# Kernel optimization log

Measured on AMD Instinct MI355X. Metric: run time of the kernel, lower is better.

## Reference

```python
import jax, jax.numpy as jnp
import numpy as np

DIM = 768
H = 12
HD = DIM // H
LAMBDA_INIT = 0.1
EPS = 1e-6


def setup_inputs() -> dict:
    key = jax.random.key(0)
    ks = jax.random.split(key, 6)
    B, N = 2, 2048
    x = jax.random.normal(ks[0], (B, N, DIM), dtype=jnp.float32)
    xpos = jnp.broadcast_to(jnp.arange(N, dtype=jnp.int64), (B, N))
    s = 1.0 / np.sqrt(DIM)
    W_qkv1 = jax.random.normal(ks[1], (DIM, 3 * DIM), dtype=jnp.float32) * s
    W_qkv2 = jax.random.normal(ks[2], (DIM, 3 * DIM), dtype=jnp.float32) * s
    W_proj = jax.random.normal(ks[3], (DIM, DIM), dtype=jnp.float32) * s
    b_proj = jnp.zeros((DIM,), dtype=jnp.float32)
    norm_w = jnp.ones((DIM,), dtype=jnp.float32)
    lambda_1 = jnp.ones((H,), dtype=jnp.float32)
    # layer_idx=0, max_layer=12 -> scale = 1/12
    lambda_2 = jnp.full((H,), 1.0 - LAMBDA_INIT * (1.0 / 12.0), dtype=jnp.float32)
    return {"x": x, "W_qkv1": W_qkv1, "W_qkv2": W_qkv2, "W_proj": W_proj,
            "b_proj": b_proj, "norm_w": norm_w, "lambda_1": lambda_1,
            "lambda_2": lambda_2, "xpos": xpos}


def _qkv(x, W):
    B, N, C = x.shape
    qkv = (x @ W).reshape(B, N, 3, H, HD).transpose(2, 0, 3, 1, 4)  # [3,B,H,N,D]
    return qkv[0], qkv[1], qkv[2]


def reference(x, W_qkv1, W_qkv2, W_proj, b_proj, norm_w, lambda_1, lambda_2, xpos):
    B, N, C = x.shape
    scale = HD ** -0.5
    q1, k1, v1 = _qkv(x, W_qkv1)
    q2, k2, v2 = _qkv(x, W_qkv2)
    attn1 = jax.nn.softmax(jnp.einsum('bhnd,bhmd->bhnm', q1, k1) * scale, axis=-1)
    attn2 = jax.nn.softmax(jnp.einsum('bhnd,bhmd->bhnm', q2, k2) * scale, axis=-1)
    lam = (lambda_1 - lambda_2 + LAMBDA_INIT)[None, :, None, None]
    diff_attn = attn1 - lam * attn2
    out = jnp.einsum('bhnm,bhmd->bhnd', diff_attn, v1)
    out = out.transpose(0, 2, 1, 3).reshape(B, N, C)
    # RMSNorm (computed in fp32, matching torch module)
    o32 = out.astype(jnp.float32)
    rms = jax.lax.rsqrt(jnp.mean(o32 * o32, axis=-1, keepdims=True) + EPS)
    out = (o32 * rms * norm_w).astype(out.dtype)
    return out @ W_proj + b_proj
```

## Files before the change

kernel.cpp:

```cpp
#include <hip/hip_runtime.h>
#include <hip/hip_bf16.h>
#include <math.h>

#define DIMC 768
#define NH   12
#define HDIM 64
#define NSEQ 2048
#define NB   2
#define LAMBDA_INIT 0.1f

typedef __attribute__((ext_vector_type(8))) short bf16x8;
typedef __attribute__((ext_vector_type(4))) float f32x4;
typedef unsigned short u16;

__device__ __forceinline__ u16 f2b(float f) {
    unsigned u = __float_as_uint(f);
    return (u16)((u + 0x7FFFu + ((u >> 16) & 1u)) >> 16);
}
__device__ __forceinline__ float b2f(u16 h) {
    return __uint_as_float((unsigned)h << 16);
}

__global__ __launch_bounds__(256)
void split32(const float* __restrict__ x, u16* __restrict__ hi,
             u16* __restrict__ lo, int n4)
{
    for (int i = blockIdx.x * 256 + threadIdx.x; i < n4; i += gridDim.x * 256) {
        float4 v = ((const float4*)x)[i];
        ushort4 h, l;
        h.x = f2b(v.x); l.x = f2b(v.x - b2f(h.x));
        h.y = f2b(v.y); l.y = f2b(v.y - b2f(h.y));
        h.z = f2b(v.z); l.z = f2b(v.z - b2f(h.z));
        h.w = f2b(v.w); l.w = f2b(v.w - b2f(h.w));
        ((ushort4*)hi)[i] = h;
        ((ushort4*)lo)[i] = l;
    }
}

__global__ __launch_bounds__(256)
void tsplit(const float* __restrict__ src, int R, int C_ld,
            u16* __restrict__ dhi, u16* __restrict__ dlo)
{
    __shared__ float T[64][65];
    const int tid = threadIdx.x;
    const int c0 = blockIdx.x * 64, r0 = blockIdx.y * 64;
    const int row = tid >> 2, cq = (tid & 3) * 4;
#pragma unroll
    for (int it = 0; it < 4; ++it) {
        int col = cq + it * 16;
        float4 v = *(const float4*)&src[(size_t)(r0 + row) * C_ld + c0 + col];
        T[row][col+0] = v.x; T[row][col+1] = v.y;
        T[row][col+2] = v.z; T[row][col+3] = v.w;
    }
    __syncthreads();
    const int c = tid >> 2, rq = (tid & 3) * 4;
#pragma unroll
    for (int it = 0; it < 4; ++it) {
        int rr = rq + it * 16;
#pragma unroll
        for (int i = 0; i < 4; ++i) {
            float f = T[rr + i][c];
            u16 h = f2b(f);
            size_t o = (size_t)(c0 + c) * R + r0 + rr + i;
            dhi[o] = h;
            dlo[o] = f2b(f - b2f(h));
        }
    }
}

template<int MODE>
__global__ __launch_bounds__(256)
void gemm_bf16(const u16* __restrict__ Ahi, const u16* __restrict__ Alo,
               const float* __restrict__ A32,
               const u16* __restrict__ Bhi, const u16* __restrict__ Blo,
               u16* __restrict__ Qo, u16* __restrict__ Ko,
               u16* __restrict__ Vhi, u16* __restrict__ Vlo,
               float* __restrict__ OUT,
               const float* __restrict__ rrms, const float* __restrict__ normw,
               const float* __restrict__ bias)
{
    __shared__ u16 AhS[128][40], AlS[128][40], BhS[128][40], BlS[128][40];
    const int tid = threadIdx.x;
    const int l = tid & 63, w = tid >> 6;
    const int wm = w >> 1, wn = w & 1;
    const int m0 = blockIdx.y * 128, n0 = blockIdx.x * 128;
    const int srow = tid >> 1, scg = (tid & 1) * 16;

    float rsc = 1.0f;
    if (MODE == 2) rsc = rrms[m0 + srow];

    f32x4 acc[4][4];
#pragma unroll
    for (int i = 0; i < 4; ++i)
#pragma unroll
        for (int j = 0; j < 4; ++j) acc[i][j] = (f32x4){0.f,0.f,0.f,0.f};

    for (int k0 = 0; k0 < DIMC; k0 += 32) {
        if (MODE < 2) {
            const u16* pa = Ahi + (size_t)(m0 + srow) * DIMC + k0 + scg;
            const u16* pl = Alo + (size_t)(m0 + srow) * DIMC + k0 + scg;
            *(bf16x8*)&AhS[srow][scg]     = *(const bf16x8*)pa;
            *(bf16x8*)&AhS[srow][scg + 8] = *(const bf16x8*)(pa + 8);
            *(bf16x8*)&AlS[srow][scg]     = *(const bf16x8*)pl;
            *(bf16x8*)&AlS[srow][scg + 8] = *(const bf16x8*)(pl + 8);
        } else {
            const float* pa = A32 + (size_t)(m0 + srow) * DIMC + k0 + scg;
            float4 v0 = *(const float4*)(pa);
            float4 v1 = *(const float4*)(pa + 4);
            float4 v2 = *(const float4*)(pa + 8);
            float4 v3 = *(const float4*)(pa + 12);
            float4 w0 = *(const float4*)(normw + k0 + scg);
            float4 w1 = *(const float4*)(normw + k0 + scg + 4);
            float4 w2 = *(const float4*)(normw + k0 + scg + 8);
            float4 w3 = *(const float4*)(normw + k0 + scg + 12);
            float vv[16] = {v0.x,v0.y,v0.z,v0.w, v1.x,v1.y,v1.z,v1.w,
                            v2.x,v2.y,v2.z,v2.w, v3.x,v3.y,v3.z,v3.w};
            float nn[16] = {w0.x,w0.y,w0.z,w0.w, w1.x,w1.y,w1.z,w1.w,
                            w2.x,w2.y,w2.z,w2.w, w3.x,w3.y,w3.z,w3.w};
#pragma unroll
            for (int i = 0; i < 16; ++i) {
                float f = vv[i] * rsc * nn[i];
                u16 h = f2b(f);
                AhS[srow][scg + i] = h;
                AlS[srow][scg + i] = f2b(f - b2f(h));
            }
        }
        {
            const u16* pb = Bhi + (size_t)(n0 + srow) * DIMC + k0 + scg;
            const u16* pl = Blo + (size_t)(n0 + srow) * DIMC + k0 + scg;
            *(bf16x8*)&BhS[srow][scg]     = *(const bf16x8*)pb;
            *(bf16x8*)&BhS[srow][scg + 8] = *(const bf16x8*)(pb + 8);
            *(bf16x8*)&BlS[srow][scg]     = *(const bf16x8*)pl;
            *(bf16x8*)&BlS[srow][scg + 8] = *(const bf16x8*)(pl + 8);
        }
        __syncthreads();

        bf16x8 ah[4], al[4], bh[4], bl[4];
#pragma unroll
        for (int i = 0; i < 4; ++i) {
            ah[i] = *(const bf16x8*)&AhS[wm*64 + i*16 + (l & 15)][(l >> 4) * 8];
            al[i] = *(const bf16x8*)&AlS[wm*64 + i*16 + (l & 15)][(l >> 4) * 8];
            bh[i] = *(const bf16x8*)&BhS[wn*64 + i*16 + (l & 15)][(l >> 4) * 8];
            bl[i] = *(const bf16x8*)&BlS[wn*64 + i*16 + (l & 15)][(l >> 4) * 8];
        }
#pragma unroll
        for (int mi = 0; mi < 4; ++mi)
#pragma unroll
            for (int ni = 0; ni < 4; ++ni) {
                acc[mi][ni] = __builtin_amdgcn_mfma_f32_16x16x32_bf16(ah[mi], bh[ni], acc[mi][ni], 0, 0, 0);
                acc[mi][ni] = __builtin_amdgcn_mfma_f32_16x16x32_bf16(ah[mi], bl[ni], acc[mi][ni], 0, 0, 0);
                acc[mi][ni] = __builtin_amdgcn_mfma_f32_16x16x32_bf16(al[mi], bh[ni], acc[mi][ni], 0, 0, 0);
            }
        __syncthreads();
    }

#pragma unroll
    for (int mi = 0; mi < 4; ++mi) {
#pragma unroll
        for (int ni = 0; ni < 4; ++ni) {
#pragma unroll
            for (int r = 0; r < 4; ++r) {
                const int m = m0 + wm*64 + mi*16 + (l >> 4) * 4 + r;
                const int n = n0 + wn*64 + ni*16 + (l & 15);
                float val = acc[mi][ni][r];
                if (MODE == 2) {
                    OUT[(size_t)m * DIMC + n] = val + bias[n];
                } else {
                    const int three = n / DIMC;
                    const int rem = n - three * DIMC;
                    const int h = rem >> 6, d = rem & 63;
                    const int b_ = m >> 11, n_ = m & (NSEQ - 1);
                    const size_t o = ((size_t)(b_ * NH + h) * NSEQ + n_) * HDIM + d;
                    if (three == 0)      Qo[o] = f2b(val * 0.125f);
                    else if (three == 1) Ko[o] = f2b(val);
                    else {
                        u16 h16 = f2b(val);
                        Vhi[o] = h16;
                        Vlo[o] = f2b(val - b2f(h16));
                    }
                }
            }
        }
    }
}

#define KVB 64
#define NT  (NSEQ / KVB)

__global__ __launch_bounds__(256)
void attn_mfma3(const u16* __restrict__ Q1, const u16* __restrict__ K1,
                const u16* __restrict__ Vhi, const u16* __restrict__ Vlo,
                const u16* __restrict__ Q2, const u16* __restrict__ K2,
                const float* __restrict__ lam1, const float* __restrict__ lam2,
                float* __restrict__ out)
{
    __shared__ u16 K1s[KVB * 64];
    __shared__ u16 K2s[KVB * 64];
    __shared__ unsigned VtHiU[64 * 36];
    __shared__ unsigned VtLoU[64 * 36];
    __shared__ unsigned PsU[2][4][16 * 36];

    const int tid = threadIdx.x;
    const int l = tid & 63, w = tid >> 6;
    const int qt = blockIdx.x, bh = blockIdx.y;
    const int b = bh / NH, h = bh % NH;
    const size_t hoff = (size_t)bh * NSEQ * HDIM;

    const int qrow = qt * 64 + w * 16 + (l & 15);
    const u16* q1p = Q1 + hoff + (size_t)qrow * HDIM + ((l >> 4) * 8);
    const u16* q2p = Q2 + hoff + (size_t)qrow * HDIM + ((l >> 4) * 8);
    bf16x8 qa1[2], qa2[2];
#pragma unroll
    for (int hf = 0; hf < 2; ++hf) {
        qa1[hf] = *(const bf16x8*)(q1p + hf * 32);
        qa2[hf] = *(const bf16x8*)(q2p + hf * 32);
    }

    f32x4 o1[4], o2[4];
    float m1[4], l1s[4], m2[4], l2s[4];
#pragma unroll
    for (int i = 0; i < 4; ++i) {
        o1[i] = (f32x4){0.f,0.f,0.f,0.f};
        o2[i] = (f32x4){0.f,0.f,0.f,0.f};
        m1[i] = -INFINITY; m2[i] = -INFINITY; l1s[i] = 0.f; l2s[i] = 0.f;
    }

    const u16* k1p = K1 + hoff;
    const u16* k2p = K2 + hoff;
    const u16* vhp = Vhi + hoff;
    const u16* vlp = Vlo + hoff;

    const int sr  = tid >> 2;
    const int scu = (tid & 3) * 16;
    const int swz = (sr & 7) << 4;
    const int vp_ = tid & 31;
    const int vdb = (tid >> 5) * 8;

    bf16x8 pk1[2], pk2[2], pvh[2], pvl[2];

#define LOADREGS(KT)                                                           \
    {                                                                          \
        const size_t gk = (size_t)((KT) * KVB + sr) * HDIM + scu;              \
        pk1[0] = *(const bf16x8*)(k1p + gk);                                   \
        pk1[1] = *(const bf16x8*)(k1p + gk + 8);                               \
        pk2[0] = *(const bf16x8*)(k2p + gk);                                   \
        pk2[1] = *(const bf16x8*)(k2p + gk + 8);                               \
        const size_t gv = (size_t)((KT) * KVB + 2 * vp_) * HDIM + vdb;         \
        pvh[0] = *(const bf16x8*)(vhp + gv);                                   \
        pvh[1] = *(const bf16x8*)(vhp + gv + HDIM);                            \
        pvl[0] = *(const bf16x8*)(vlp + gv);                                   \
        pvl[1] = *(const bf16x8*)(vlp + gv + HDIM);                            \
    }

    LOADREGS(0)

    for (int kt = 0; kt < NT; ++kt) {
        __syncthreads();
#pragma unroll
        for (int i = 0; i < 2; ++i) {
            const int bc = (scu + i * 8) * 2;
            *(bf16x8*)((char*)K1s + sr * 128 + (bc ^ swz)) = pk1[i];
            *(bf16x8*)((char*)K2s + sr * 128 + (bc ^ swz)) = pk2[i];
        }
#pragma unroll
        for (int j = 0; j < 8; ++j) {
            VtHiU[(vdb + j) * 36 + vp_] =
                (unsigned)(u16)pvh[0][j] | ((unsigned)(u16)pvh[1][j] << 16);
            VtLoU[(vdb + j) * 36 + vp_] =
                (unsigned)(u16)pvl[0][j] | ((unsigned)(u16)pvl[1][j] << 16);
        }
        __syncthreads();

        if (kt + 1 < NT) LOADREGS(kt + 1)

        f32x4 s1[4], s2[4];
#pragma unroll
        for (int s = 0; s < 4; ++s) {
            s1[s] = (f32x4){0.f,0.f,0.f,0.f};
            s2[s] = (f32x4){0.f,0.f,0.f,0.f};
        }
        const int xr = (l & 7) << 4;
#pragma unroll
        for (int hf = 0; hf < 2; ++hf) {
            const int d0b = ((l >> 4) << 4) + (hf << 6);
#pragma unroll
            for (int s = 0; s < 4; ++s) {
                const int ra = s * 16 + (l & 15);
                bf16x8 kb1 = *(const bf16x8*)((const char*)K1s + ra * 128 + (d0b ^ xr));
                bf16x8 kb2 = *(const bf16x8*)((const char*)K2s + ra * 128 + (d0b ^ xr));
                s1[s] = __builtin_amdgcn_mfma_f32_16x16x32_bf16(qa1[hf], kb1, s1[s], 0, 0, 0);
                s2[s] = __builtin_amdgcn_mfma_f32_16x16x32_bf16(qa2[hf], kb2, s2[s], 0, 0, 0);
            }
        }

        unsigned* pw1 = &PsU[0][w][0];
        unsigned* pw2 = &PsU[1][w][0];
#pragma unroll
        for (int r = 0; r < 4; ++r) {
            const int row = (l >> 4) * 4 + r;
            float rm1 = fmaxf(fmaxf(s1[0][r], s1[1][r]), fmaxf(s1[2][r], s1[3][r]));
            float rm2 = fmaxf(fmaxf(s2[0][r], s2[1][r]), fmaxf(s2[2][r], s2[3][r]));
#pragma unroll
            for (int mm = 1; mm < 16; mm <<= 1) {
                rm1 = fmaxf(rm1, __shfl_xor(rm1, mm));
                rm2 = fmaxf(rm2, __shfl_xor(rm2, mm));
            }
            float mn1 = fmaxf(m1[r], rm1), mn2 = fmaxf(m2[r], rm2);
            float c1 = __expf(m1[r] - mn1), c2 = __expf(m2[r] - mn2);
            u16 h1[4], h2v[4];
            float rs1 = 0.f, rs2 = 0.f;
#pragma unroll
            for (int s = 0; s < 4; ++s) {
                h1[s]  = f2b(__expf(s1[s][r] - mn1));
                h2v[s] = f2b(__expf(s2[s][r] - mn2));
                rs1 += b2f(h1[s]);
                rs2 += b2f(h2v[s]);
            }
#pragma unroll
            for (int mm = 1; mm < 16; mm <<= 1) {
                rs1 += __shfl_xor(rs1, mm);
                rs2 += __shfl_xor(rs2, mm);
            }
            l1s[r] = l1s[r] * c1 + rs1;  m1[r] = mn1;
            l2s[r] = l2s[r] * c2 + rs2;  m2[r] = mn2;
#pragma unroll
            for (int dt = 0; dt < 4; ++dt) { o1[dt][r] *= c1; o2[dt][r] *= c2; }

            int x1[4], x2[4];
#pragma unroll
            for (int s = 0; s < 4; ++s) {
                x1[s] = __shfl_xor((int)h1[s], 1);
                x2[s] = __shfl_xor((int)h2v[s], 1);
            }
            const int u = l & 15;
            if ((l & 1) == 0) {
                pw1[row*36 +      (u >> 1)] = (unsigned)h1[0]  | ((unsigned)x1[0] << 16);
                pw1[row*36 + 16 + (u >> 1)] = (unsigned)h1[2]  | ((unsigned)x1[2] << 16);
                pw2[row*36 +      (u >> 1)] = (unsigned)h2v[0] | ((unsigned)x2[0] << 16);
                pw2[row*36 + 16 + (u >> 1)] = (unsigned)h2v[2] | ((unsigned)x2[2] << 16);
            } else {
                pw1[row*36 +  8 + (u >> 1)] = (unsigned)x1[1]  | ((unsigned)h1[1] << 16);
                pw1[row*36 + 24 + (u >> 1)] = (unsigned)x1[3]  | ((unsigned)h1[3] << 16);
                pw2[row*36 +  8 + (u >> 1)] = (unsigned)x2[1]  | ((unsigned)h2v[1] << 16);
                pw2[row*36 + 24 + (u >> 1)] = (unsigned)x2[3]  | ((unsigned)h2v[3] << 16);
            }
        }

#pragma unroll
        for (int h2 = 0; h2 < 2; ++h2) {
            const int po = (l & 15) * 144 + h2 * 64 + ((l >> 4) << 4);
            bf16x8 pa = *(const bf16x8*)((const char*)pw1 + po);
            bf16x8 pb = *(const bf16x8*)((const char*)pw2 + po);
#pragma unroll
            for (int dt = 0; dt < 4; ++dt) {
                const int vo = (dt * 16 + (l & 15)) * 144 + h2 * 64 + ((l >> 4) << 4);
                bf16x8 vhib = *(const bf16x8*)((const char*)VtHiU + vo);
                bf16x8 vlob = *(const bf16x8*)((const char*)VtLoU + vo);
                o1[dt] = __builtin_amdgcn_mfma_f32_16x16x32_bf16(pa, vhib, o1[dt], 0, 0, 0);
                o1[dt] = __builtin_amdgcn_mfma_f32_16x16x32_bf16(pa, vlob, o1[dt], 0, 0, 0);
                o2[dt] = __builtin_amdgcn_mfma_f32_16x16x32_bf16(pb, vhib, o2[dt], 0, 0, 0);
                o2[dt] = __builtin_amdgcn_mfma_f32_16x16x32_bf16(pb, vlob, o2[dt], 0, 0, 0);
            }
        }
    }
#undef LOADREGS

    const float lam = lam1[h] - lam2[h] + LAMBDA_INIT;
#pragma unroll
    for (int r = 0; r < 4; ++r) {
        const float i1 = 1.0f / l1s[r];
        const float i2 = lam / l2s[r];
        const int q = qt * 64 + w * 16 + (l >> 4) * 4 + r;
        const size_t rowoff = (size_t)(b * NSEQ + q) * DIMC + h * HDIM;
#pragma unroll
        for (int dt = 0; dt < 4; ++dt)
            out[rowoff + dt * 16 + (l & 15)] = o1[dt][r] * i1 - o2[dt][r] * i2;
    }
}

__global__ __launch_bounds__(256)
void rrms_kernel(const float* __restrict__ X, float* __restrict__ R)
{
    const int r = blockIdx.x;
    const int t = threadIdx.x;
    const float* row = X + (size_t)r * DIMC;
    float s = 0.f;
#pragma unroll
    for (int k = 0; k < 3; ++k) {
        float v = row[t + k * 256];
        s = fmaf(v, v, s);
    }
#pragma unroll
    for (int mm = 1; mm < 64; mm <<= 1) s += __shfl_xor(s, mm);
    __shared__ float wsum[4];
    if ((t & 63) == 0) wsum[t >> 6] = s;
    __syncthreads();
    if (t == 0) R[r] = rsqrtf((wsum[0]+wsum[1]+wsum[2]+wsum[3]) * (1.0f/DIMC) + 1e-6f);
}

extern "C" void kernel_launch(void* const* d_in, const int* in_sizes, int n_in,
                              void* d_out, int out_size, void* d_ws, size_t ws_size,
                              hipStream_t stream)
{
    const float* x   = (const float*)d_in[0];
    const float* Wq1 = (const float*)d_in[1];
    const float* Wq2 = (const float*)d_in[2];
    const float* Wp  = (const float*)d_in[3];
    const float* bp  = (const float*)d_in[4];
    const float* nw  = (const float*)d_in[5];
    const float* la1 = (const float*)d_in[6];
    const float* la2 = (const float*)d_in[7];
    float* out = (float*)d_out;

    const size_t HSZ = (size_t)NB * NH * NSEQ * HDIM;
    const size_t XSZ = (size_t)NB * NSEQ * DIMC;

    u16* p = (u16*)d_ws;
    u16* Q1b = p;  p += HSZ;
    u16* K1b = p;  p += HSZ;
    u16* Q2b = p;  p += HSZ;
    u16* K2b = p;  p += HSZ;
    u16* V1h = p;  p += HSZ;
    u16* V1l = p;  p += HSZ;
    u16* xhi = p;  p += XSZ;
    u16* xlo = p;  p += XSZ;
    u16* W1th = p; p += (size_t)2304 * 768;
    u16* W1tl = p; p += (size_t)2304 * 768;
    u16* W2th = p; p += (size_t)1536 * 768;
    u16* W2tl = p; p += (size_t)1536 * 768;
    u16* Wpth = p; p += (size_t)768 * 768;
    u16* Wptl = p; p += (size_t)768 * 768;
    float* AO = (float*)p;
    float* RR = AO + XSZ;

    split32<<<dim3(1024), 256, 0, stream>>>(x, xhi, xlo, (int)(XSZ / 4));
    tsplit<<<dim3(36, 12), 256, 0, stream>>>(Wq1, DIMC, 3*DIMC, W1th, W1tl);
    tsplit<<<dim3(24, 12), 256, 0, stream>>>(Wq2, DIMC, 3*DIMC, W2th, W2tl);
    tsplit<<<dim3(12, 12), 256, 0, stream>>>(Wp,  DIMC, DIMC,   Wpth, Wptl);

    gemm_bf16<0><<<dim3(18, 32), 256, 0, stream>>>(xhi, xlo, nullptr, W1th, W1tl,
                                                   Q1b, K1b, V1h, V1l, nullptr,
                                                   nullptr, nullptr, nullptr);
    gemm_bf16<1><<<dim3(12, 32), 256, 0, stream>>>(xhi, xlo, nullptr, W2th, W2tl,
                                                   Q2b, K2b, nullptr, nullptr, nullptr,
                                                   nullptr, nullptr, nullptr);
    attn_mfma3<<<dim3(NSEQ/64, NB*NH), 256, 0, stream>>>(Q1b, K1b, V1h, V1l,
                                                         Q2b, K2b, la1, la2, AO);
    rrms_kernel<<<dim3(NB*NSEQ), 256, 0, stream>>>(AO, RR);
    gemm_bf16<2><<<dim3(6, 32), 256, 0, stream>>>(nullptr, nullptr, AO, Wpth, Wptl,
                                                  nullptr, nullptr, nullptr, nullptr,
                                                  out, RR, nw, bp);
}
```

Baseline: 523.1 us.

## Split the two attention branches across separate wave groups in a 512-thread block

Result: faster. 492.8 us (-5.8%).

```diff
diff --git a/kernel.cpp b/kernel.cpp
--- a/kernel.cpp
+++ b/kernel.cpp
@@ -187,42 +187,41 @@
 #define KVB 64
 #define NT  (NSEQ / KVB)
 
-__global__ __launch_bounds__(256)
-void attn_mfma3(const u16* __restrict__ Q1, const u16* __restrict__ K1,
+__global__ __launch_bounds__(512)
+void attn_mfma4(const u16* __restrict__ Q1, const u16* __restrict__ K1,
                 const u16* __restrict__ Vhi, const u16* __restrict__ Vlo,
                 const u16* __restrict__ Q2, const u16* __restrict__ K2,
                 const float* __restrict__ lam1, const float* __restrict__ lam2,
                 float* __restrict__ out)
 {
-    __shared__ u16 K1s[KVB * 64];
-    __shared__ u16 K2s[KVB * 64];
-    __shared__ unsigned VtHiU[64 * 36];
-    __shared__ unsigned VtLoU[64 * 36];
-    __shared__ unsigned PsU[2][4][16 * 36];
+    __shared__ char SMEM[53248];
+    u16*      K1s   = (u16*)SMEM;
+    u16*      K2s   = (u16*)(SMEM + 8192);
+    unsigned* VtHiU = (unsigned*)(SMEM + 16384);
+    unsigned* VtLoU = (unsigned*)(SMEM + 25600);
+    unsigned* PsU   = (unsigned*)(SMEM + 34816);
 
     const int tid = threadIdx.x;
     const int l = tid & 63, w = tid >> 6;
+    const int branch = w >> 2;
+    const int g = w & 3;
     const int qt = blockIdx.x, bh = blockIdx.y;
     const int b = bh / NH, h = bh % NH;
     const size_t hoff = (size_t)bh * NSEQ * HDIM;
 
-    const int qrow = qt * 64 + w * 16 + (l & 15);
-    const u16* q1p = Q1 + hoff + (size_t)qrow * HDIM + ((l >> 4) * 8);
-    const u16* q2p = Q2 + hoff + (size_t)qrow * HDIM + ((l >> 4) * 8);
-    bf16x8 qa1[2], qa2[2];
-#pragma unroll
-    for (int hf = 0; hf < 2; ++hf) {
-        qa1[hf] = *(const bf16x8*)(q1p + hf * 32);
-        qa2[hf] = *(const bf16x8*)(q2p + hf * 32);
-    }
-
-    f32x4 o1[4], o2[4];
-    float m1[4], l1s[4], m2[4], l2s[4];
+    const u16* qbase = branch ? Q2 : Q1;
+    const int qrow = qt * 64 + g * 16 + (l & 15);
+    const u16* qp = qbase + hoff + (size_t)qrow * HDIM + ((l >> 4) * 8);
+    bf16x8 qa[2];
+    qa[0] = *(const bf16x8*)(qp);
+    qa[1] = *(const bf16x8*)(qp + 32);
+
+    f32x4 o[4];
+    float m[4], ls[4];
 #pragma unroll
     for (int i = 0; i < 4; ++i) {
-        o1[i] = (f32x4){0.f,0.f,0.f,0.f};
-        o2[i] = (f32x4){0.f,0.f,0.f,0.f};
-        m1[i] = -INFINITY; m2[i] = -INFINITY; l1s[i] = 0.f; l2s[i] = 0.f;
+        o[i] = (f32x4){0.f,0.f,0.f,0.f};
+        m[i] = -INFINITY; ls[i] = 0.f;
     }
 
     const u16* k1p = K1 + hoff;
@@ -230,151 +229,144 @@
     const u16* vhp = Vhi + hoff;
     const u16* vlp = Vlo + hoff;
 
-    const int sr  = tid >> 2;
-    const int scu = (tid & 3) * 16;
+    const int sr  = tid >> 3;
+    const int scu = (tid & 7) * 8;
     const int swz = (sr & 7) << 4;
     const int vp_ = tid & 31;
-    const int vdb = (tid >> 5) * 8;
-
-    bf16x8 pk1[2], pk2[2], pvh[2], pvl[2];
+    const int vdb = (tid >> 5) * 4;
+
+    bf16x8 pk1, pk2;
+    ushort4 pvh[2], pvl[2];
 
 #define LOADREGS(KT)                                                           \
     {                                                                          \
         const size_t gk = (size_t)((KT) * KVB + sr) * HDIM + scu;              \
-        pk1[0] = *(const bf16x8*)(k1p + gk);                                   \
-        pk1[1] = *(const bf16x8*)(k1p + gk + 8);                               \
-        pk2[0] = *(const bf16x8*)(k2p + gk);                                   \
-        pk2[1] = *(const bf16x8*)(k2p + gk + 8);                               \
+        pk1 = *(const bf16x8*)(k1p + gk);                                      \
+        pk2 = *(const bf16x8*)(k2p + gk);                                      \
         const size_t gv = (size_t)((KT) * KVB + 2 * vp_) * HDIM + vdb;         \
-        pvh[0] = *(const bf16x8*)(vhp + gv);                                   \
-        pvh[1] = *(const bf16x8*)(vhp + gv + HDIM);                            \
-        pvl[0] = *(const bf16x8*)(vlp + gv);                                   \
-        pvl[1] = *(const bf16x8*)(vlp + gv + HDIM);                            \
+        pvh[0] = *(const ushort4*)(vhp + gv);                                  \
+        pvh[1] = *(const ushort4*)(vhp + gv + HDIM);                           \
+        pvl[0] = *(const ushort4*)(vlp + gv);                                  \
+        pvl[1] = *(const ushort4*)(vlp + gv + HDIM);                           \
     }
 
     LOADREGS(0)
+
+    const char* kb = branch ? (const char*)K2s : (const char*)K1s;
+    unsigned* pw = &PsU[w * 576];
 
     for (int kt = 0; kt < NT; ++kt) {
         __syncthreads();
-#pragma unroll
-        for (int i = 0; i < 2; ++i) {
-            const int bc = (scu + i * 8) * 2;
-            *(bf16x8*)((char*)K1s + sr * 128 + (bc ^ swz)) = pk1[i];
-            *(bf16x8*)((char*)K2s + sr * 128 + (bc ^ swz)) = pk2[i];
-        }
-#pragma unroll
-        for (int j = 0; j < 8; ++j) {
-            VtHiU[(vdb + j) * 36 + vp_] =
-                (unsigned)(u16)pvh[0][j] | ((unsigned)(u16)pvh[1][j] << 16);
-            VtLoU[(vdb + j) * 36 + vp_] =
-                (unsigned)(u16)pvl[0][j] | ((unsigned)(u16)pvl[1][j] << 16);
+        *(bf16x8*)((char*)K1s + sr * 128 + ((scu * 2) ^ swz)) = pk1;
+        *(bf16x8*)((char*)K2s + sr * 128 + ((scu * 2) ^ swz)) = pk2;
+        {
+            unsigned hv0[4] = {pvh[0].x, pvh[0].y, pvh[0].z, pvh[0].w};
+            unsigned hv1[4] = {pvh[1].x, pvh[1].y, pvh[1].z, pvh[1].w};
+            unsigned lv0[4] = {pvl[0].x, pvl[0].y, pvl[0].z, pvl[0].w};
+            unsigned lv1[4] = {pvl[1].x, pvl[1].y, pvl[1].z, pvl[1].w};
+#pragma unroll
+            for (int j = 0; j < 4; ++j) {
+                VtHiU[(vdb + j) * 36 + vp_] = hv0[j] | (hv1[j] << 16);
+                VtLoU[(vdb + j) * 36 + vp_] = lv0[j] | (lv1[j] << 16);
+            }
         }
         __syncthreads();
 
         if (kt + 1 < NT) LOADREGS(kt + 1)
 
-        f32x4 s1[4], s2[4];
-#pragma unroll
-        for (int s = 0; s < 4; ++s) {
-            s1[s] = (f32x4){0.f,0.f,0.f,0.f};
-            s2[s] = (f32x4){0.f,0.f,0.f,0.f};
-        }
+        f32x4 s[4];
+#pragma unroll
+        for (int si = 0; si < 4; ++si) s[si] = (f32x4){0.f,0.f,0.f,0.f};
         const int xr = (l & 7) << 4;
 #pragma unroll
         for (int hf = 0; hf < 2; ++hf) {
             const int d0b = ((l >> 4) << 4) + (hf << 6);
 #pragma unroll
-            for (int s = 0; s < 4; ++s) {
-                const int ra = s * 16 + (l & 15);
-                bf16x8 kb1 = *(const bf16x8*)((const char*)K1s + ra * 128 + (d0b ^ xr));
-                bf16x8 kb2 = *(const bf16x8*)((const char*)K2s + ra * 128 + (d0b ^ xr));
-                s1[s] = __builtin_amdgcn_mfma_f32_16x16x32_bf16(qa1[hf], kb1, s1[s], 0, 0, 0);
-                s2[s] = __builtin_amdgcn_mfma_f32_16x16x32_bf16(qa2[hf], kb2, s2[s], 0, 0, 0);
-            }
-        }
-
-        unsigned* pw1 = &PsU[0][w][0];
-        unsigned* pw2 = &PsU[1][w][0];
+            for (int si = 0; si < 4; ++si) {
+                const int ra = si * 16 + (l & 15);
+                bf16x8 kv = *(const bf16x8*)(kb + ra * 128 + (d0b ^ xr));
+                s[si] = __builtin_amdgcn_mfma_f32_16x16x32_bf16(qa[hf], kv, s[si], 0, 0, 0);
+            }
+        }
+
 #pragma unroll
         for (int r = 0; r < 4; ++r) {
             const int row = (l >> 4) * 4 + r;
-            float rm1 = fmaxf(fmaxf(s1[0][r], s1[1][r]), fmaxf(s1[2][r], s1[3][r]));
-            float rm2 = fmaxf(fmaxf(s2[0][r], s2[1][r]), fmaxf(s2[2][r], s2[3][r]));
-#pragma unroll
-            for (int mm = 1; mm < 16; mm <<= 1) {
-                rm1 = fmaxf(rm1, __shfl_xor(rm1, mm));
-                rm2 = fmaxf(rm2, __shfl_xor(rm2, mm));
-            }
-            float mn1 = fmaxf(m1[r], rm1), mn2 = fmaxf(m2[r], rm2);
-            float c1 = __expf(m1[r] - mn1), c2 = __expf(m2[r] - mn2);
-            u16 h1[4], h2v[4];
-            float rs1 = 0.f, rs2 = 0.f;
-#pragma unroll
-            for (int s = 0; s < 4; ++s) {
-                h1[s]  = f2b(__expf(s1[s][r] - mn1));
-                h2v[s] = f2b(__expf(s2[s][r] - mn2));
-                rs1 += b2f(h1[s]);
-                rs2 += b2f(h2v[s]);
-            }
-#pragma unroll
-            for (int mm = 1; mm < 16; mm <<= 1) {
-                rs1 += __shfl_xor(rs1, mm);
-                rs2 += __shfl_xor(rs2, mm);
-            }
-            l1s[r] = l1s[r] * c1 + rs1;  m1[r] = mn1;
-            l2s[r] = l2s[r] * c2 + rs2;  m2[r] = mn2;
-#pragma unroll
-            for (int dt = 0; dt < 4; ++dt) { o1[dt][r] *= c1; o2[dt][r] *= c2; }
-
-            int x1[4], x2[4];
-#pragma unroll
-            for (int s = 0; s < 4; ++s) {
-                x1[s] = __shfl_xor((int)h1[s], 1);
-                x2[s] = __shfl_xor((int)h2v[s], 1);
-            }
+            float rm = fmaxf(fmaxf(s[0][r], s[1][r]), fmaxf(s[2][r], s[3][r]));
+#pragma unroll
+            for (int mm = 1; mm < 16; mm <<= 1)
+                rm = fmaxf(rm, __shfl_xor(rm, mm));
+            float mn = fmaxf(m[r], rm);
+            float c = __expf(m[r] - mn);
+            u16 hh[4];
+            float rs = 0.f;
+#pragma unroll
+            for (int si = 0; si < 4; ++si) {
+                hh[si] = f2b(__expf(s[si][r] - mn));
+                rs += b2f(hh[si]);
+            }
+#pragma unroll
+            for (int mm = 1; mm < 16; mm <<= 1)
+                rs += __shfl_xor(rs, mm);
+            ls[r] = ls[r] * c + rs;  m[r] = mn;
+#pragma unroll
+            for (int dt = 0; dt < 4; ++dt) o[dt][r] *= c;
+
+            int xx[4];
+#pragma unroll
+            for (int si = 0; si < 4; ++si) xx[si] = __shfl_xor((int)hh[si], 1);
             const int u = l & 15;
             if ((l & 1) == 0) {
-                pw1[row*36 +      (u >> 1)] = (unsigned)h1[0]  | ((unsigned)x1[0] << 16);
-                pw1[row*36 + 16 + (u >> 1)] = (unsigned)h1[2]  | ((unsigned)x1[2] << 16);
-                pw2[row*36 +      (u >> 1)] = (unsigned)h2v[0] | ((unsigned)x2[0] << 16);
-                pw2[row*36 + 16 + (u >> 1)] = (unsigned)h2v[2] | ((unsigned)x2[2] << 16);
+                pw[row*36 +      (u >> 1)] = (unsigned)hh[0] | ((unsigned)xx[0] << 16);
+                pw[row*36 + 16 + (u >> 1)] = (unsigned)hh[2] | ((unsigned)xx[2] << 16);
             } else {
-                pw1[row*36 +  8 + (u >> 1)] = (unsigned)x1[1]  | ((unsigned)h1[1] << 16);
-                pw1[row*36 + 24 + (u >> 1)] = (unsigned)x1[3]  | ((unsigned)h1[3] << 16);
-                pw2[row*36 +  8 + (u >> 1)] = (unsigned)x2[1]  | ((unsigned)h2v[1] << 16);
-                pw2[row*36 + 24 + (u >> 1)] = (unsigned)x2[3]  | ((unsigned)h2v[3] << 16);
+                pw[row*36 +  8 + (u >> 1)] = (unsigned)xx[1] | ((unsigned)hh[1] << 16);
+                pw[row*36 + 24 + (u >> 1)] = (unsigned)xx[3] | ((unsigned)hh[3] << 16);
             }
         }
 
 #pragma unroll
         for (int h2 = 0; h2 < 2; ++h2) {
             const int po = (l & 15) * 144 + h2 * 64 + ((l >> 4) << 4);
-            bf16x8 pa = *(const bf16x8*)((const char*)pw1 + po);
-            bf16x8 pb = *(const bf16x8*)((const char*)pw2 + po);
+            bf16x8 pa = *(const bf16x8*)((const char*)pw + po);
 #pragma unroll
             for (int dt = 0; dt < 4; ++dt) {
                 const int vo = (dt * 16 + (l & 15)) * 144 + h2 * 64 + ((l >> 4) << 4);
                 bf16x8 vhib = *(const bf16x8*)((const char*)VtHiU + vo);
                 bf16x8 vlob = *(const bf16x8*)((const char*)VtLoU + vo);
-                o1[dt] = __builtin_amdgcn_mfma_f32_16x16x32_bf16(pa, vhib, o1[dt], 0, 0, 0);
-                o1[dt] = __builtin_amdgcn_mfma_f32_16x16x32_bf16(pa, vlob, o1[dt], 0, 0, 0);
-                o2[dt] = __builtin_amdgcn_mfma_f32_16x16x32_bf16(pb, vhib, o2[dt], 0, 0, 0);
-                o2[dt] = __builtin_amdgcn_mfma_f32_16x16x32_bf16(pb, vlob, o2[dt], 0, 0, 0);
+                o[dt] = __builtin_amdgcn_mfma_f32_16x16x32_bf16(pa, vhib, o[dt], 0, 0, 0);
+                o[dt] = __builtin_amdgcn_mfma_f32_16x16x32_bf16(pa, vlob, o[dt], 0, 0, 0);
             }
         }
     }
 #undef LOADREGS
 
-    const float lam = lam1[h] - lam2[h] + LAMBDA_INIT;
-#pragma unroll
-    for (int r = 0; r < 4; ++r) {
-        const float i1 = 1.0f / l1s[r];
-        const float i2 = lam / l2s[r];
-        const int q = qt * 64 + w * 16 + (l >> 4) * 4 + r;
-        const size_t rowoff = (size_t)(b * NSEQ + q) * DIMC + h * HDIM;
-#pragma unroll
-        for (int dt = 0; dt < 4; ++dt)
-            out[rowoff + dt * 16 + (l & 15)] = o1[dt][r] * i1 - o2[dt][r] * i2;
+    __syncthreads();
+    float* MRG = (float*)SMEM;
+    if (branch == 1) {
+        const float lam = lam1[h] - lam2[h] + LAMBDA_INIT;
+#pragma unroll
+        for (int r = 0; r < 4; ++r) {
+            const float i2 = lam / ls[r];
+            const int row = (l >> 4) * 4 + r;
+#pragma unroll
+            for (int dt = 0; dt < 4; ++dt)
+                MRG[(g * 16 + row) * 68 + dt * 16 + (l & 15)] = o[dt][r] * i2;
+        }
+    }
+    __syncthreads();
+    if (branch == 0) {
+#pragma unroll
+        for (int r = 0; r < 4; ++r) {
+            const float i1 = 1.0f / ls[r];
+            const int row = (l >> 4) * 4 + r;
+            const int q = qt * 64 + g * 16 + row;
+            const size_t rowoff = (size_t)(b * NSEQ + q) * DIMC + h * HDIM;
+#pragma unroll
+            for (int dt = 0; dt < 4; ++dt)
+                out[rowoff + dt * 16 + (l & 15)] =
+                    o[dt][r] * i1 - MRG[(g * 16 + row) * 68 + dt * 16 + (l & 15)];
+        }
     }
 }
 
@@ -444,7 +436,7 @@
     gemm_bf16<1><<<dim3(12, 32), 256, 0, stream>>>(xhi, xlo, nullptr, W2th, W2tl,
                                                    Q2b, K2b, nullptr, nullptr, nullptr,
                                                    nullptr, nullptr, nullptr);
-    attn_mfma3<<<dim3(NSEQ/64, NB*NH), 256, 0, stream>>>(Q1b, K1b, V1h, V1l,
+    attn_mfma4<<<dim3(NSEQ/64, NB*NH), 512, 0, stream>>>(Q1b, K1b, V1h, V1l,
                                                          Q2b, K2b, la1, la2, AO);
     rrms_kernel<<<dim3(NB*NSEQ), 256, 0, stream>>>(AO, RR);
     gemm_bf16<2><<<dim3(6, 32), 256, 0, stream>>>(nullptr, nullptr, AO, Wpth, Wptl,
```
